# Optimization experiments

Measured on AMD Instinct MI355X. Metric: run time of the kernel, lower is better.

Reference implementation:

```python
import jax, jax.numpy as jnp
import numpy as np

NH, WIN = 8, 7  # num_head, window


def _ln(x, w, b, eps=1e-6):
    mu = x.mean(-1, keepdims=True)
    var = ((x - mu) ** 2).mean(-1, keepdims=True)
    return (x - mu) / jnp.sqrt(var + eps) * w + b


def _dwconv(x, w, b):
    # x: (B,C,H,W), w: (C,1,7,7) depthwise, pad 3
    y = jax.lax.conv_general_dilated(
        x, w, (1, 1), ((3, 3), (3, 3)),
        dimension_numbers=('NCHW', 'OIHW', 'NCHW'),
        feature_group_count=x.shape[1])
    return y + b[None, :, None, None]


def _forward(x, x_e, norm_w, norm_b, norme_w, norme_b,
             rr1_w, rr1_b, rr2_w, rr2_b, rr3_w, rr3_b, conv_w, conv_b,
             la1_w, la1_b, la2_w, la2_b, lac1_w, lac1_b, lac2_w, lac2_b,
             fc1_w, fc2_w, la3_w, la3_b,
             kv_w, kv_b, q_w, q_b, proj_w, proj_b, proje_w, proje_b):
    B, H, W, C = x.shape
    hd = C // NH // 2  # head dim of half-width attention
    xn = _ln(x, norm_w, norm_b)
    xen = _ln(x_e, norme_w, norme_b)

    # local_rr branch: gated depthwise-conv mixing (C channels)
    rr1 = xn @ rr1_w + rr1_b
    rr2 = xn @ rr2_w + rr2_b
    rr2 = _dwconv(rr2.transpose(0, 3, 1, 2), conv_w, conv_b).transpose(0, 2, 3, 1)
    rr2 = rr2 @ rr3_w + rr3_b
    local_rr = rr1 * rr2  # (B,H,W,C)

    # LocalAttentionRGBT branch -> (B,H,W,C//2)
    rgb = (xn @ la1_w + la1_b).transpose(0, 3, 1, 2)   # (B,C/2,H,W)
    t = (xen @ la2_w + la2_b).transpose(0, 3, 1, 2)
    co = _dwconv(rgb * t, lac1_w, lac1_b)
    di = _dwconv(jnp.abs(rgb - t), lac2_w, lac2_b)
    co_di = jnp.concatenate([co, di], 1).transpose(0, 2, 3, 1)  # (B,H,W,C)
    amap = co_di.mean(-1, keepdims=True)                         # (B,H,W,1)
    dot = (amap * co_di).sum((1, 2), keepdims=True)              # (B,1,1,C)
    n1 = jnp.sqrt((amap ** 2).sum((1, 2), keepdims=True))        # (B,1,1,1)
    n2 = jnp.sqrt((co_di ** 2).sum((1, 2), keepdims=True))       # (B,1,1,C)
    cos = dot / (n1 * n2 + 1e-6)
    attc = jax.nn.sigmoid(jax.nn.gelu(cos @ fc1_w, approximate=False) @ fc2_w)
    local_rx = (co_di * attc) @ la3_w + la3_b  # (B,H,W,C/2)

    # global pooled attention: 49 queries vs full H*W keys, C/2 wide
    kv = (xn @ kv_w + kv_b).reshape(B, H * W, 2, NH, hd).transpose(2, 0, 3, 1, 4)
    k, v = kv[0], kv[1]  # (B,NH,HW,hd)
    rx = jnp.concatenate([xn, xen], -1)  # (B,H,W,3C/2)
    ph, pw = H // WIN, W // WIN  # exact adaptive pool (H,W divisible by 7)
    rx_pool = rx.reshape(B, WIN, ph, WIN, pw, rx.shape[-1]).mean((2, 4))  # (B,7,7,3C/2)
    q = (rx_pool @ q_w + q_b).reshape(B, WIN * WIN, NH, hd).transpose(0, 2, 1, 3)
    attn = jax.nn.softmax((q * hd ** -0.5) @ k.transpose(0, 1, 3, 2), axis=-1)  # (B,NH,49,HW)
    g = (attn @ v).reshape(B, NH, WIN, WIN, hd).transpose(0, 1, 4, 2, 3).reshape(B, C // 2, WIN, WIN)
    g = jax.image.resize(g, (B, C // 2, H, W), method='bilinear').transpose(0, 2, 3, 1)

    xc = jnp.concatenate([local_rr, g, local_rx], -1)  # (B,H,W,2C)
    out_e = xc @ proje_w + proje_b  # (B,H,W,C/2)
    out = xc @ proj_w + proj_b      # (B,H,W,C)
    return out, out_e


def setup_inputs() -> dict:
    C = 128
    B, H, W = 8, 112, 112
    ks = iter(jax.random.split(jax.random.key(0), 24))

    def w(shape):
        return jax.random.normal(next(ks), shape, jnp.float32) * 0.05

    inp = {
        'x': jax.random.normal(next(ks), (B, H, W, C), jnp.float32),
        'x_e': jax.random.normal(next(ks), (B, H, W, C // 2), jnp.float32),
        'norm_w': jnp.ones((C,), jnp.float32), 'norm_b': jnp.zeros((C,), jnp.float32),
        'norme_w': jnp.ones((C // 2,), jnp.float32), 'norme_b': jnp.zeros((C // 2,), jnp.float32),
        'rr1_w': w((C, C)), 'rr1_b': jnp.zeros((C,), jnp.float32),
        'rr2_w': w((C, C)), 'rr2_b': jnp.zeros((C,), jnp.float32),
        'rr3_w': w((C, C)), 'rr3_b': jnp.zeros((C,), jnp.float32),
        'conv_w': w((C, 1, 7, 7)), 'conv_b': jnp.zeros((C,), jnp.float32),
        'la1_w': w((C, C // 2)), 'la1_b': jnp.zeros((C // 2,), jnp.float32),
        'la2_w': w((C // 2, C // 2)), 'la2_b': jnp.zeros((C // 2,), jnp.float32),
        'lac1_w': w((C // 2, 1, 7, 7)), 'lac1_b': jnp.zeros((C // 2,), jnp.float32),
        'lac2_w': w((C // 2, 1, 7, 7)), 'lac2_b': jnp.zeros((C // 2,), jnp.float32),
        'fc1_w': w((C, C // 8)), 'fc2_w': w((C // 8, C)),
        'la3_w': w((C, C // 2)), 'la3_b': jnp.zeros((C // 2,), jnp.float32),
        'kv_w': w((C, C)), 'kv_b': jnp.zeros((C,), jnp.float32),
        'q_w': w((3 * C // 2, C // 2)), 'q_b': jnp.zeros((C // 2,), jnp.float32),
        'proj_w': w((2 * C, C)), 'proj_b': jnp.zeros((C,), jnp.float32),
        'proje_w': w((2 * C, C // 2)), 'proje_b': jnp.zeros((C // 2,), jnp.float32),
    }
    return inp


def reference(x, x_e, norm_w, norm_b, norme_w, norme_b,
              rr1_w, rr1_b, rr2_w, rr2_b, rr3_w, rr3_b, conv_w, conv_b,
              la1_w, la1_b, la2_w, la2_b, lac1_w, lac1_b, lac2_w, lac2_b,
              fc1_w, fc2_w, la3_w, la3_b,
              kv_w, kv_b, q_w, q_b, proj_w, proj_b, proje_w, proje_b):
    return _forward(x, x_e, norm_w, norm_b, norme_w, norme_b,
                    rr1_w, rr1_b, rr2_w, rr2_b, rr3_w, rr3_b, conv_w, conv_b,
                    la1_w, la1_b, la2_w, la2_b, lac1_w, lac1_b, lac2_w, lac2_b,
                    fc1_w, fc2_w, la3_w, la3_b,
                    kv_w, kv_b, q_w, q_b, proj_w, proj_b, proje_w, proje_b)
```

## Files before the change

kernel.cpp:

```cpp
#include <hip/hip_runtime.h>
#include <math.h>

#define N_POS 100352
#define HW    12544

typedef unsigned short bf16_t;
typedef __attribute__((ext_vector_type(8))) short bf16x8;
typedef __attribute__((ext_vector_type(4))) float f32x4;

__device__ __forceinline__ bf16_t f2b(float f){
  unsigned u = __builtin_bit_cast(unsigned, f);
  unsigned r = (u + 0x7fffu + ((u >> 16) & 1u)) >> 16;
  return (bf16_t)r;
}
__device__ __forceinline__ float b2f(bf16_t h){
  unsigned u = ((unsigned)h) << 16;
  return __builtin_bit_cast(float, u);
}
__device__ __forceinline__ float blo(unsigned u){
  return __builtin_bit_cast(float, u << 16);
}
__device__ __forceinline__ float bhi(unsigned u){
  return __builtin_bit_cast(float, u & 0xffff0000u);
}

__global__ void zero_kernel(float* p, int n){
  int i = blockIdx.x*256 + threadIdx.x;
  if (i < n) p[i] = 0.f;
}

struct WJob { const float* src; bf16_t* dst; int K; int ldw; int n0; };
struct WJobs { WJob j[14]; };
__global__ void wtrans_kernel(WJobs js){
  WJob job = js.j[blockIdx.x];
  int t = threadIdx.x;
  int n = t & 63, k0 = t >> 6;
  for (int k = k0; k < job.K; k += 4)
    job.dst[(size_t)n*job.K + k] = f2b(job.src[(size_t)k*job.ldw + job.n0 + n]);
}

__global__ __launch_bounds__(256) void ln128_kernel(const float* __restrict__ in,
    const float* __restrict__ w, const float* __restrict__ b, bf16_t* __restrict__ out){
  int row  = blockIdx.x*4 + (threadIdx.x >> 6);
  int lane = threadIdx.x & 63;
  const float* p = in + (size_t)row*128;
  float2 v = *(const float2*)(p + lane*2);
  float s = v.x + v.y;
  #pragma unroll
  for (int o = 1; o < 64; o <<= 1) s += __shfl_xor(s, o);
  float mu = s * (1.0f/128.0f);
  float dx = v.x - mu, dy = v.y - mu;
  float q = dx*dx + dy*dy;
  #pragma unroll
  for (int o = 1; o < 64; o <<= 1) q += __shfl_xor(q, o);
  float rs = rsqrtf(q * (1.0f/128.0f) + 1e-6f);
  int c = lane*2;
  ushort2 o2;
  o2.x = f2b(dx*rs*w[c]   + b[c]);
  o2.y = f2b(dy*rs*w[c+1] + b[c+1]);
  *(ushort2*)(out + (size_t)row*128 + c) = o2;
}

__global__ __launch_bounds__(256) void ln64_kernel(const float* __restrict__ in,
    const float* __restrict__ w, const float* __restrict__ b, bf16_t* __restrict__ out){
  int row  = blockIdx.x*4 + (threadIdx.x >> 6);
  int lane = threadIdx.x & 63;
  float v = in[(size_t)row*64 + lane];
  float s = v;
  #pragma unroll
  for (int o = 1; o < 64; o <<= 1) s += __shfl_xor(s, o);
  float mu = s * (1.0f/64.0f);
  float d = v - mu;
  float q = d*d;
  #pragma unroll
  for (int o = 1; o < 64; o <<= 1) q += __shfl_xor(q, o);
  float rs = rsqrtf(q * (1.0f/64.0f) + 1e-6f);
  out[(size_t)row*64 + lane] = f2b(d*rs*w[lane] + b[lane]);
}

struct MTile {
  const bf16_t* Wt;
  const float* bias;
  void* out;
  const bf16_t* mult;
  int ldo; int ldm; int out_fp32;
};
struct MGemmParams {
  const bf16_t* A; const float* scale;
  int lda; int K; int rowsPerB; int ntiles;
  MTile tiles[8];
};

__global__ __launch_bounds__(256) void mgemm(MGemmParams p){
  __shared__ short As[128*72];
  __shared__ short Ws[64*72];
  const int tid = threadIdx.x;
  const int bid = blockIdx.x;
  const int xcd = bid & 7;
  const int j = bid >> 3;
  const int ti = j % p.ntiles;
  const int rb = (j / p.ntiles) * 8 + xcd;
  const MTile tile = p.tiles[ti];
  const int row0 = rb * 128;
  const int lane = tid & 63, wv = tid >> 6;
  const int wm = wv * 32;
  const int fm = lane & 15;
  const int quad = lane >> 4;
  f32x4 acc[2][4];
  #pragma unroll
  for (int mi = 0; mi < 2; mi++)
    #pragma unroll
    for (int ni = 0; ni < 4; ni++) acc[mi][ni] = (f32x4)0.f;
  const float* scale = p.scale ? (p.scale + (size_t)(row0 / p.rowsPerB) * p.K) : (const float*)0;

  const int sr = tid & 127, sq = tid >> 7;
  const int wn = tid & 63,  wq = tid >> 6;

  for (int k0 = 0; k0 < p.K; k0 += 64) {
    {
      const bf16_t* src = p.A + (size_t)(row0 + sr)*p.lda + k0 + sq*32;
      short* dst = &As[sr*72 + sq*32];
      if (!scale) {
        #pragma unroll
        for (int i = 0; i < 4; i++)
          *(uint4*)(dst + i*8) = *(const uint4*)(src + i*8);
      } else {
        const float* sc = scale + k0 + sq*32;
        #pragma unroll
        for (int i = 0; i < 32; i++) dst[i] = (short)f2b(b2f(src[i]) * sc[i]);
      }
    }
    {
      const bf16_t* src = tile.Wt + (size_t)wn*p.K + k0 + wq*16;
      short* dst = &Ws[wn*72 + wq*16];
      *(uint4*)dst       = *(const uint4*)src;
      *(uint4*)(dst + 8) = *(const uint4*)(src + 8);
    }
    __syncthreads();
    #pragma unroll
    for (int ks = 0; ks < 2; ks++) {
      int kb = ks*32 + quad*8;
      bf16x8 af0 = *(const bf16x8*)&As[(wm + fm)*72 + kb];
      bf16x8 af1 = *(const bf16x8*)&As[(wm + 16 + fm)*72 + kb];
      bf16x8 bfr[4];
      #pragma unroll
      for (int ni = 0; ni < 4; ni++) bfr[ni] = *(const bf16x8*)&Ws[(ni*16 + fm)*72 + kb];
      #pragma unroll
      for (int ni = 0; ni < 4; ni++) {
        acc[0][ni] = __builtin_amdgcn_mfma_f32_16x16x32_bf16(af0, bfr[ni], acc[0][ni], 0, 0, 0);
        acc[1][ni] = __builtin_amdgcn_mfma_f32_16x16x32_bf16(af1, bfr[ni], acc[1][ni], 0, 0, 0);
      }
    }
    __syncthreads();
  }
  #pragma unroll
  for (int mi = 0; mi < 2; mi++) {
    #pragma unroll
    for (int ni = 0; ni < 4; ni++) {
      int col = ni*16 + fm;
      float bias = tile.bias[col];
      #pragma unroll
      for (int r = 0; r < 4; r++) {
        int row = row0 + wm + mi*16 + quad*4 + r;
        float val = acc[mi][ni][r] + bias;
        if (tile.mult) val *= b2f(tile.mult[(size_t)row*tile.ldm + col]);
        if (tile.out_fp32) ((float*)tile.out)[(size_t)row*tile.ldo + col] = val;
        else ((bf16_t*)tile.out)[(size_t)row*tile.ldo + col] = f2b(val);
      }
    }
  }
}

__global__ __launch_bounds__(256) void dwconv128_kernel(const bf16_t* __restrict__ in,
    const float* __restrict__ cw, const float* __restrict__ cb, bf16_t* __restrict__ out){
  __shared__ float wsm[49*128];
  int t = threadIdx.x;
  for (int i = t; i < 6272; i += 256) {
    int ch = i & 127, k = i >> 7;
    wsm[k*128 + ch] = cw[ch*49 + k];
  }
  __syncthreads();
  int c = (t & 63) * 2;
  int wv = t >> 6;
  int blk = blockIdx.x;
  int xs = blk % 14; int tmp = blk / 14;
  int yg = tmp % 14; int b = tmp / 14;
  int y0 = yg*8 + wv*2;
  int x0 = xs*8;
  float2 bias; bias.x = cb[c]; bias.y = cb[c+1];
  float2 acc0[8], acc1[8];
  #pragma unroll
  for (int i = 0; i < 8; i++) { acc0[i] = bias; acc1[i] = bias; }
  for (int r = 0; r < 8; r++) {
    int yy = y0 + r - 3;
    if ((unsigned)yy >= 112u) continue;
    const bf16_t* row = in + ((size_t)(b*112+yy)*112)*128 + c;
    unsigned u[14];
    #pragma unroll
    for (int i = 0; i < 14; i++) {
      int xx = x0 + i - 3;
      u[i] = ((unsigned)xx < 112u) ? *(const unsigned*)(row + (size_t)xx*128) : 0u;
    }
    float va[14], vb[14];
    #pragma unroll
    for (int i = 0; i < 14; i++) { va[i] = blo(u[i]); vb[i] = bhi(u[i]); }
    if (r < 7) {
      #pragma unroll
      for (int kx = 0; kx < 7; kx++) {
        float2 w = *(const float2*)&wsm[(r*7+kx)*128 + c];
        #pragma unroll
        for (int i = 0; i < 8; i++) {
          acc0[i].x = fmaf(w.x, va[i+kx], acc0[i].x);
          acc0[i].y = fmaf(w.y, vb[i+kx], acc0[i].y);
        }
      }
    }
    if (r >= 1) {
      #pragma unroll
      for (int kx = 0; kx < 7; kx++) {
        float2 w = *(const float2*)&wsm[((r-1)*7+kx)*128 + c];
        #pragma unroll
        for (int i = 0; i < 8; i++) {
          acc1[i].x = fmaf(w.x, va[i+kx], acc1[i].x);
          acc1[i].y = fmaf(w.y, vb[i+kx], acc1[i].y);
        }
      }
    }
  }
  size_t r0 = (size_t)(b*112+y0)*112 + x0;
  #pragma unroll
  for (int i = 0; i < 8; i++) {
    unsigned o0 = (unsigned)f2b(acc0[i].x) | ((unsigned)f2b(acc0[i].y) << 16);
    unsigned o1 = (unsigned)f2b(acc1[i].x) | ((unsigned)f2b(acc1[i].y) << 16);
    *(unsigned*)(out + (r0+i)*128 + c)       = o0;
    *(unsigned*)(out + (r0+112+i)*128 + c)   = o1;
  }
}

__global__ __launch_bounds__(256) void dwconv_codi_kernel(
    const bf16_t* __restrict__ rgb, const bf16_t* __restrict__ tb,
    const float* __restrict__ w1, const float* __restrict__ b1,
    const float* __restrict__ w2, const float* __restrict__ b2,
    bf16_t* __restrict__ out){
  __shared__ float wsm[49*128];
  int t = threadIdx.x;
  for (int i = t; i < 3136; i += 256) {
    int ch = i & 63, k = i >> 6;
    wsm[k*128 + ch]      = w1[ch*49 + k];
    wsm[k*128 + 64 + ch] = w2[ch*49 + k];
  }
  __syncthreads();
  int c = (t & 31) * 2;
  int wv = t >> 5;
  int blk = blockIdx.x;
  int xs = blk % 14; int tmp = blk / 14;
  int yg = tmp % 7; int b = tmp / 7;
  int y0 = yg*16 + wv*2;
  int x0 = xs*8;
  float2 bco; bco.x = b1[c]; bco.y = b1[c+1];
  float2 bdi; bdi.x = b2[c]; bdi.y = b2[c+1];
  float2 aco0[8], aco1[8], adi0[8], adi1[8];
  #pragma unroll
  for (int i = 0; i < 8; i++) { aco0[i] = bco; aco1[i] = bco; adi0[i] = bdi; adi1[i] = bdi; }
  for (int r = 0; r < 8; r++) {
    int yy = y0 + r - 3;
    if ((unsigned)yy >= 112u) continue;
    const bf16_t* rrow = rgb + ((size_t)(b*112+yy)*112)*64 + c;
    const bf16_t* trow = tb  + ((size_t)(b*112+yy)*112)*64 + c;
    unsigned ru[14], tu[14];
    #pragma unroll
    for (int i = 0; i < 14; i++) {
      int xx = x0 + i - 3;
      bool ok = (unsigned)xx < 112u;
      ru[i] = ok ? *(const unsigned*)(rrow + (size_t)xx*64) : 0u;
      tu[i] = ok ? *(const unsigned*)(trow + (size_t)xx*64) : 0u;
    }
    float p0[14], p1[14], d0[14], d1[14];
    #pragma unroll
    for (int i = 0; i < 14; i++) {
      float a0 = blo(ru[i]), a1 = bhi(ru[i]);
      float t0 = blo(tu[i]), t1 = bhi(tu[i]);
      p0[i] = a0*t0; p1[i] = a1*t1;
      d0[i] = fabsf(a0-t0); d1[i] = fabsf(a1-t1);
    }
    if (r < 7) {
      #pragma unroll
      for (int kx = 0; kx < 7; kx++) {
        int k = r*7+kx;
        float2 wc = *(const float2*)&wsm[k*128 + c];
        float2 wd = *(const float2*)&wsm[k*128 + 64 + c];
        #pragma unroll
        for (int i = 0; i < 8; i++) {
          aco0[i].x = fmaf(wc.x, p0[i+kx], aco0[i].x);
          aco0[i].y = fmaf(wc.y, p1[i+kx], aco0[i].y);
          adi0[i].x = fmaf(wd.x, d0[i+kx], adi0[i].x);
          adi0[i].y = fmaf(wd.y, d1[i+kx], adi0[i].y);
        }
      }
    }
    if (r >= 1) {
      #pragma unroll
      for (int kx = 0; kx < 7; kx++) {
        int k = (r-1)*7+kx;
        float2 wc = *(const float2*)&wsm[k*128 + c];
        float2 wd = *(const float2*)&wsm[k*128 + 64 + c];
        #pragma unroll
        for (int i = 0; i < 8; i++) {
          aco1[i].x = fmaf(wc.x, p0[i+kx], aco1[i].x);
          aco1[i].y = fmaf(wc.y, p1[i+kx], aco1[i].y);
          adi1[i].x = fmaf(wd.x, d0[i+kx], adi1[i].x);
          adi1[i].y = fmaf(wd.y, d1[i+kx], adi1[i].y);
        }
      }
    }
  }
  size_t r0 = (size_t)(b*112+y0)*112 + x0;
  #pragma unroll
  for (int i = 0; i < 8; i++) {
    unsigned oc0 = (unsigned)f2b(aco0[i].x) | ((unsigned)f2b(aco0[i].y) << 16);
    unsigned od0 = (unsigned)f2b(adi0[i].x) | ((unsigned)f2b(adi0[i].y) << 16);
    unsigned oc1 = (unsigned)f2b(aco1[i].x) | ((unsigned)f2b(aco1[i].y) << 16);
    unsigned od1 = (unsigned)f2b(adi1[i].x) | ((unsigned)f2b(adi1[i].y) << 16);
    *(unsigned*)(out + (r0+i)*128 + c)            = oc0;
    *(unsigned*)(out + (r0+i)*128 + 64 + c)       = od0;
    *(unsigned*)(out + (r0+112+i)*128 + c)        = oc1;
    *(unsigned*)(out + (r0+112+i)*128 + 64 + c)   = od1;
  }
}

__global__ __launch_bounds__(256) void reduce_kernel(const bf16_t* __restrict__ codi,
    float* __restrict__ dotb, float* __restrict__ n1sq, float* __restrict__ n2sq){
  int blk = blockIdx.x;
  int b = blk / 49, seg = blk % 49;
  int lane = threadIdx.x & 63, w = threadIdx.x >> 6;
  int c = lane*2;
  float d0=0,d1=0,s0=0,s1=0,a1=0;
  for (int i = 0; i < 64; i++) {
    int row = b*HW + seg*256 + w*64 + i;
    ushort2 v2 = *(const ushort2*)(codi + (size_t)row*128 + c);
    float vx = b2f(v2.x), vy = b2f(v2.y);
    float rs = vx + vy;
    #pragma unroll
    for (int o = 1; o < 64; o <<= 1) rs += __shfl_xor(rs, o);
    float amap = rs * (1.0f/128.0f);
    d0 += amap*vx; d1 += amap*vy;
    s0 += vx*vx;   s1 += vy*vy;
    if (lane == 0) a1 += amap*amap;
  }
  atomicAdd(&dotb[b*128+c],   d0); atomicAdd(&dotb[b*128+c+1], d1);
  atomicAdd(&n2sq[b*128+c],   s0); atomicAdd(&n2sq[b*128+c+1], s1);
  if (lane == 0) atomicAdd(&n1sq[b], a1);
}

__global__ __launch_bounds__(128) void attc_kernel(const float* __restrict__ dotb,
    const float* __restrict__ n1sq, const float* __restrict__ n2sq,
    const float* __restrict__ fc1, const float* __restrict__ fc2, float* __restrict__ attc){
  __shared__ float scos[128];
  __shared__ float sh[16];
  int t = threadIdx.x;
  int b = blockIdx.x;
  {
    float n1 = sqrtf(n1sq[b]);
    float n2 = sqrtf(n2sq[b*128+t]);
    scos[t] = dotb[b*128+t] / (n1*n2 + 1e-6f);
  }
  __syncthreads();
  if (t < 16) {
    float h = 0;
    for (int c = 0; c < 128; c++) h += scos[c]*fc1[c*16+t];
    sh[t] = h * 0.5f * (1.0f + erff(h*0.70710678118654752f));
  }
  __syncthreads();
  {
    float a = 0;
    for (int j = 0; j < 16; j++) a += sh[j]*fc2[j*128+t];
    attc[b*128+t] = 1.0f/(1.0f + __expf(-a));
  }
}

__global__ void pool_kernel(const bf16_t* __restrict__ xn, const bf16_t* __restrict__ xen,
                            float* __restrict__ pool){
  int cellb = blockIdx.x;
  int py = blockIdx.y;
  int c = threadIdx.x;
  int b = cellb / 49, cell = cellb % 49;
  int wy = cell / 7, wx = cell % 7;
  float s = 0;
  for (int i = py*2; i < py*2+2; i++)
    for (int j = 0; j < 16; j++) {
      int y = wy*16+i, x = wx*16+j;
      size_t row = (size_t)(b*112+y)*112 + x;
      s += (c < 128) ? b2f(xn[row*128 + c]) : b2f(xen[row*64 + (c-128)]);
    }
  atomicAdd(&pool[(size_t)cellb*192 + c], s);
}

__global__ void qproj_kernel(const float* __restrict__ pool, const float* __restrict__ qw,
                             const float* __restrict__ qb, float* __restrict__ qbuf){
  int cellb = blockIdx.x;
  int j = threadIdx.x;
  float s = qb[j];
  for (int c = 0; c < 192; c++)
    s += pool[(size_t)cellb*192 + c] * (1.0f/256.0f) * qw[c*64 + j];
  qbuf[(size_t)cellb*64 + j] = s * 0.35355339059327373f;
}

__global__ __launch_bounds__(256) void attn_kernel(const float* __restrict__ qbuf,
    const bf16_t* __restrict__ kv, float* __restrict__ part){
  __shared__ float qs[392];
  __shared__ float ks[256*8];
  __shared__ float vs[256*8];
  int t = threadIdx.x;
  int blk = blockIdx.x;
  int b = blk >> 7, nh = (blk >> 4) & 7, sp = blk & 15;
  for (int i = t; i < 392; i += 256)
    qs[i] = qbuf[(size_t)(b*49 + (i>>3))*64 + nh*8 + (i&7)];
  __syncthreads();
  int lane = t & 63, w = t >> 6;
  int qq = lane < 49 ? lane : 0;
  float4 qa = *(const float4*)&qs[qq*8];
  float4 qb4 = *(const float4*)&qs[qq*8+4];
  float m = -1e30f, l = 0.f;
  float4 acca = make_float4(0,0,0,0), accb = make_float4(0,0,0,0);
  const int base = sp * 784;
  uint4 kr, vr;
  {
    size_t rb = ((size_t)(b*HW + base + t))*128 + nh*8;
    kr = *(const uint4*)(kv + rb);
    vr = *(const uint4*)(kv + rb + 64);
  }
  for (int c0 = 0; c0 < 784; c0 += 256) {
    int cnt = 784 - c0 < 256 ? 784 - c0 : 256;
    __syncthreads();
    if (t < cnt) {
      const bf16_t* kp = (const bf16_t*)&kr;
      const bf16_t* vp = (const bf16_t*)&vr;
      float4 k0 = make_float4(b2f(kp[0]), b2f(kp[1]), b2f(kp[2]), b2f(kp[3]));
      float4 k1 = make_float4(b2f(kp[4]), b2f(kp[5]), b2f(kp[6]), b2f(kp[7]));
      float4 v0 = make_float4(b2f(vp[0]), b2f(vp[1]), b2f(vp[2]), b2f(vp[3]));
      float4 v1 = make_float4(b2f(vp[4]), b2f(vp[5]), b2f(vp[6]), b2f(vp[7]));
      *(float4*)&ks[t*8]   = k0; *(float4*)&ks[t*8+4] = k1;
      *(float4*)&vs[t*8]   = v0; *(float4*)&vs[t*8+4] = v1;
    }
    __syncthreads();
    int c1 = c0 + 256;
    if (c1 < 784) {
      int cnt1 = 784 - c1 < 256 ? 784 - c1 : 256;
      if (t < cnt1) {
        size_t rb = ((size_t)(b*HW + base + c1 + t))*128 + nh*8;
        kr = *(const uint4*)(kv + rb);
        vr = *(const uint4*)(kv + rb + 64);
      }
    }
    int s0 = w*64;
    int n = cnt - s0; if (n < 0) n = 0; if (n > 64) n = 64;
    for (int i = 0; i < n; i += 16) {
      float s[16];
      #pragma unroll
      for (int j = 0; j < 16; j++) {
        const float* kp = &ks[(s0+i+j)*8];
        float4 ka = *(const float4*)kp, kb = *(const float4*)(kp+4);
        s[j] = qa.x*ka.x + qa.y*ka.y + qa.z*ka.z + qa.w*ka.w
             + qb4.x*kb.x + qb4.y*kb.y + qb4.z*kb.z + qb4.w*kb.w;
      }
      float t8[8];
      #pragma unroll
      for (int j = 0; j < 8; j++) t8[j] = fmaxf(s[2*j], s[2*j+1]);
      float t4a = fmaxf(t8[0], t8[1]), t4b = fmaxf(t8[2], t8[3]);
      float t4c = fmaxf(t8[4], t8[5]), t4d = fmaxf(t8[6], t8[7]);
      float mx = fmaxf(fmaxf(t4a, t4b), fmaxf(t4c, t4d));
      float mn = fmaxf(m, mx);
      float corr = __expf(m - mn);
      float p[16];
      #pragma unroll
      for (int j = 0; j < 16; j++) p[j] = __expf(s[j] - mn);
      float u8[8];
      #pragma unroll
      for (int j = 0; j < 8; j++) u8[j] = p[2*j] + p[2*j+1];
      float u4a = u8[0]+u8[1], u4b = u8[2]+u8[3], u4c = u8[4]+u8[5], u4d = u8[6]+u8[7];
      float lsum = (u4a+u4b) + (u4c+u4d);
      l = fmaf(l, corr, lsum);
      float4 sva = make_float4(0,0,0,0), svb = make_float4(0,0,0,0);
      #pragma unroll
      for (int j = 0; j < 16; j++) {
        const float* vp = &vs[(s0+i+j)*8];
        float4 va = *(const float4*)vp, vb = *(const float4*)(vp+4);
        sva.x = fmaf(p[j], va.x, sva.x); sva.y = fmaf(p[j], va.y, sva.y);
        sva.z = fmaf(p[j], va.z, sva.z); sva.w = fmaf(p[j], va.w, sva.w);
        svb.x = fmaf(p[j], vb.x, svb.x); svb.y = fmaf(p[j], vb.y, svb.y);
        svb.z = fmaf(p[j], vb.z, svb.z); svb.w = fmaf(p[j], vb.w, svb.w);
      }
      acca.x = fmaf(acca.x, corr, sva.x); acca.y = fmaf(acca.y, corr, sva.y);
      acca.z = fmaf(acca.z, corr, sva.z); acca.w = fmaf(acca.w, corr, sva.w);
      accb.x = fmaf(accb.x, corr, svb.x); accb.y = fmaf(accb.y, corr, svb.y);
      accb.z = fmaf(accb.z, corr, svb.z); accb.w = fmaf(accb.w, corr, svb.w);
      m = mn;
    }
  }
  __syncthreads();
  if (lane < 49) {
    float* rp = &vs[((size_t)w*49 + lane)*10];
    rp[0] = m; rp[1] = l;
    rp[2] = acca.x; rp[3] = acca.y; rp[4] = acca.z; rp[5] = acca.w;
    rp[6] = accb.x; rp[7] = accb.y; rp[8] = accb.z; rp[9] = accb.w;
  }
  __syncthreads();
  if (t < 49) {
    float M = -1e30f;
    #pragma unroll
    for (int w4 = 0; w4 < 4; w4++) M = fmaxf(M, vs[(w4*49 + t)*10]);
    float L = 0, a[8] = {0,0,0,0,0,0,0,0};
    #pragma unroll
    for (int w4 = 0; w4 < 4; w4++) {
      const float* rp = &vs[(w4*49 + t)*10];
      float c = __expf(rp[0] - M);
      L += rp[1]*c;
      #pragma unroll
      for (int d = 0; d < 8; d++) a[d] += rp[2+d]*c;
    }
    size_t idx = ((size_t)blk*49 + t)*10;
    part[idx] = M; part[idx+1] = L;
    #pragma unroll
    for (int d = 0; d < 8; d++) part[idx+2+d] = a[d];
  }
}

__global__ void merge_kernel(const float* __restrict__ part, float* __restrict__ gsm){
  int g = blockIdx.x*64 + threadIdx.x;
  if (g >= 3136) return;
  int b = g / 392, r = g % 392, nh = r / 49, q = r % 49;
  int blkbase = b*128 + nh*16;
  float M = -1e30f;
  for (int sp = 0; sp < 16; sp++)
    M = fmaxf(M, part[((size_t)(blkbase+sp)*49 + q)*10]);
  float L = 0, a[8] = {0,0,0,0,0,0,0,0};
  for (int sp = 0; sp < 16; sp++) {
    size_t idx = ((size_t)(blkbase+sp)*49 + q)*10;
    float c = __expf(part[idx] - M);
    L += part[idx+1]*c;
    #pragma unroll
    for (int d = 0; d < 8; d++) a[d] += part[idx+2+d]*c;
  }
  #pragma unroll
  for (int d = 0; d < 8; d++)
    gsm[(size_t)(b*49+q)*64 + nh*8 + d] = a[d]/L;
}

__global__ __launch_bounds__(256) void f2_kernel(const float* __restrict__ gsm,
                                                 bf16_t* __restrict__ xc){
  int gidx = blockIdx.x*256 + threadIdx.x;
  int r = gidx >> 6, cc = gidx & 63;
  int b = r / HW, rem = r % HW, y = rem / 112, x = rem % 112;
  float fy = fminf(fmaxf((y + 0.5f)*0.0625f - 0.5f, 0.f), 6.f);
  float fx = fminf(fmaxf((x + 0.5f)*0.0625f - 0.5f, 0.f), 6.f);
  int y0 = (int)fy, x0 = (int)fx;
  float wy = fy - y0, wx = fx - x0;
  int y1 = y0+1 < 6 ? y0+1 : 6, x1 = x0+1 < 6 ? x0+1 : 6;
  const float* gb = gsm + (size_t)b*49*64 + cc;
  float g00 = gb[(y0*7+x0)*64], g01 = gb[(y0*7+x1)*64];
  float g10 = gb[(y1*7+x0)*64], g11 = gb[(y1*7+x1)*64];
  xc[(size_t)r*256 + 128 + cc] =
      f2b((1-wy)*((1-wx)*g00 + wx*g01) + wy*((1-wx)*g10 + wx*g11));
}

extern "C" void kernel_launch(void* const* d_in, const int* in_sizes, int n_in,
                              void* d_out, int out_size, void* d_ws, size_t ws_size,
                              hipStream_t stream) {
  const float* x      = (const float*)d_in[0];
  const float* x_e    = (const float*)d_in[1];
  const float* norm_w = (const float*)d_in[2];
  const float* norm_b = (const float*)d_in[3];
  const float* norme_w= (const float*)d_in[4];
  const float* norme_b= (const float*)d_in[5];
  const float* rr1_w  = (const float*)d_in[6];
  const float* rr1_b  = (const float*)d_in[7];
  const float* rr2_w  = (const float*)d_in[8];
  const float* rr2_b  = (const float*)d_in[9];
  const float* rr3_w  = (const float*)d_in[10];
  const float* rr3_b  = (const float*)d_in[11];
  const float* conv_w = (const float*)d_in[12];
  const float* conv_b = (const float*)d_in[13];
  const float* la1_w  = (const float*)d_in[14];
  const float* la1_b  = (const float*)d_in[15];
  const float* la2_w  = (const float*)d_in[16];
  const float* la2_b  = (const float*)d_in[17];
  const float* lac1_w = (const float*)d_in[18];
  const float* lac1_b = (const float*)d_in[19];
  const float* lac2_w = (const float*)d_in[20];
  const float* lac2_b = (const float*)d_in[21];
  const float* fc1_w  = (const float*)d_in[22];
  const float* fc2_w  = (const float*)d_in[23];
  const float* la3_w  = (const float*)d_in[24];
  const float* la3_b  = (const float*)d_in[25];
  const float* kv_w   = (const float*)d_in[26];
  const float* kv_b   = (const float*)d_in[27];
  const float* q_w    = (const float*)d_in[28];
  const float* q_b    = (const float*)d_in[29];
  const float* proj_w = (const float*)d_in[30];
  const float* proj_b = (const float*)d_in[31];
  const float* proje_w= (const float*)d_in[32];
  const float* proje_b= (const float*)d_in[33];

  const size_t N = N_POS;
  bf16_t* rr1   = (bf16_t*)d_ws;
  bf16_t* xnbuf = rr1 + N*128;
  bf16_t* kvbuf = xnbuf + N*128;
  bf16_t* xcbuf = kvbuf + N*128;
  float* pool = (float*)(xcbuf + N*256);
  float* qbuf = pool + 75264;
  float* part = qbuf + 25088;
  float* gsm  = part + 1003520;
  float* dotb = gsm  + 25088;
  float* n1sq = dotb + 1024;
  float* n2sq = n1sq + 8;
  float* attc = n2sq + 1024;
  bf16_t* wtab = (bf16_t*)(attc + 1024);

  bf16_t* xn = xnbuf;
  bf16_t* convout = xnbuf;
  bf16_t* kv = kvbuf;
  bf16_t* codi = kvbuf;
  bf16_t* rr2a = xcbuf;
  bf16_t* rgb  = xcbuf + N*128;
  bf16_t* xen  = xcbuf + N*192;
  bf16_t* xc   = xcbuf;
  float* outp = (float*)d_out;
  float* oute = outp + N*128;

  bf16_t* rr1t0 = wtab;            bf16_t* rr1t1 = wtab + 8192;
  bf16_t* rr2t0 = wtab + 16384;    bf16_t* rr2t1 = wtab + 24576;
  bf16_t* la1t  = wtab + 32768;
  bf16_t* kvt0  = wtab + 40960;    bf16_t* kvt1  = wtab + 49152;
  bf16_t* la2t  = wtab + 57344;
  bf16_t* rr3t0 = wtab + 61440;    bf16_t* rr3t1 = wtab + 69632;
  bf16_t* la3t  = wtab + 77824;
  bf16_t* projt0= wtab + 86016;    bf16_t* projt1= wtab + 102400;
  bf16_t* projet= wtab + 118784;

  zero_kernel<<<(75264+255)/256, 256, 0, stream>>>(pool, 75264);
  zero_kernel<<<9, 256, 0, stream>>>(dotb, 2056);
  {
    WJobs js;
    js.j[0]  = {rr1_w,  rr1t0, 128, 128,   0};
    js.j[1]  = {rr1_w,  rr1t1, 128, 128,  64};
    js.j[2]  = {rr2_w,  rr2t0, 128, 128,   0};
    js.j[3]  = {rr2_w,  rr2t1, 128, 128,  64};
    js.j[4]  = {la1_w,  la1t,  128,  64,   0};
    js.j[5]  = {kv_w,   kvt0,  128, 128,   0};
    js.j[6]  = {kv_w,   kvt1,  128, 128,  64};
    js.j[7]  = {la2_w,  la2t,   64,  64,   0};
    js.j[8]  = {rr3_w,  rr3t0, 128, 128,   0};
    js.j[9]  = {rr3_w,  rr3t1, 128, 128,  64};
    js.j[10] = {la3_w,  la3t,  128,  64,   0};
    js.j[11] = {proj_w, projt0,256, 128,   0};
    js.j[12] = {proj_w, projt1,256, 128,  64};
    js.j[13] = {proje_w,projet,256,  64,   0};
    wtrans_kernel<<<14, 256, 0, stream>>>(js);
  }
  ln128_kernel<<<N_POS/4, 256, 0, stream>>>(x, norm_w, norm_b, xn);
  ln64_kernel <<<N_POS/4, 256, 0, stream>>>(x_e, norme_w, norme_b, xen);
  pool_kernel<<<dim3(392,8), 192, 0, stream>>>(xn, xen, pool);
  qproj_kernel<<<392, 64, 0, stream>>>(pool, q_w, q_b, qbuf);
  {
    MGemmParams p; p.A = xn; p.scale = 0; p.lda = 128; p.K = 128; p.rowsPerB = HW; p.ntiles = 7;
    p.tiles[0] = {rr1t0, rr1_b,    rr1,     0, 128, 0, 0};
    p.tiles[1] = {rr1t1, rr1_b+64, rr1+64,  0, 128, 0, 0};
    p.tiles[2] = {rr2t0, rr2_b,    rr2a,    0, 128, 0, 0};
    p.tiles[3] = {rr2t1, rr2_b+64, rr2a+64, 0, 128, 0, 0};
    p.tiles[4] = {la1t,  la1_b,    rgb,     0,  64, 0, 0};
    p.tiles[5] = {kvt0,  kv_b,     kv,      0, 128, 0, 0};
    p.tiles[6] = {kvt1,  kv_b+64,  kv+64,   0, 128, 0, 0};
    mgemm<<<8*7*98, 256, 0, stream>>>(p);
  }
  attn_kernel<<<1024, 256, 0, stream>>>(qbuf, kv, part);
  merge_kernel<<<49, 64, 0, stream>>>(part, gsm);
  {
    MGemmParams p; p.A = xen; p.scale = 0; p.lda = 64; p.K = 64; p.rowsPerB = HW; p.ntiles = 1;
    p.tiles[0] = {la2t, la2_b, xen, 0, 64, 0, 0};
    mgemm<<<8*1*98, 256, 0, stream>>>(p);
  }
  dwconv_codi_kernel<<<8*7*14, 256, 0, stream>>>(rgb, xen, lac1_w, lac1_b, lac2_w, lac2_b, codi);
  dwconv128_kernel<<<8*14*14, 256, 0, stream>>>(rr2a, conv_w, conv_b, convout);
  {
    MGemmParams p; p.A = convout; p.scale = 0; p.lda = 128; p.K = 128; p.rowsPerB = HW; p.ntiles = 2;
    p.tiles[0] = {rr3t0, rr3_b,    xc,    rr1,    256, 128, 0};
    p.tiles[1] = {rr3t1, rr3_b+64, xc+64, rr1+64, 256, 128, 0};
    mgemm<<<8*2*98, 256, 0, stream>>>(p);
  }
  reduce_kernel<<<392, 256, 0, stream>>>(codi, dotb, n1sq, n2sq);
  attc_kernel<<<8, 128, 0, stream>>>(dotb, n1sq, n2sq, fc1_w, fc2_w, attc);
  {
    MGemmParams p; p.A = codi; p.scale = attc; p.lda = 128; p.K = 128; p.rowsPerB = HW; p.ntiles = 1;
    p.tiles[0] = {la3t, la3_b, xc + 192, 0, 256, 0, 0};
    mgemm<<<8*1*98, 256, 0, stream>>>(p);
  }
  f2_kernel<<<25088, 256, 0, stream>>>(gsm, xc);
  {
    MGemmParams p; p.A = xc; p.scale = 0; p.lda = 256; p.K = 256; p.rowsPerB = HW; p.ntiles = 3;
    p.tiles[0] = {projt0, proj_b,    outp,    0, 128, 0, 1};
    p.tiles[1] = {projt1, proj_b+64, outp+64, 0, 128, 0, 1};
    p.tiles[2] = {projet, proje_b,   oute,    0,  64, 0, 1};
    mgemm<<<8*3*98, 256, 0, stream>>>(p);
  }
}
```

Baseline: 596.3 us.

## Keep A row-block resident in LDS and loop over N tiles per block

The multi-tile GEMM becomes a templated kernel in which each block loads its full-K A row block into shared memory once and then iterates over all output column tiles. Previously each block handled one tile and reloaded A for every tile. The next weight chunk is prefetched into registers while MFMAs run on the current one, and K and the tile sizes are now compile-time constants. In exchange each block does more serial work, the grid is smaller, and larger LDS use may limit occupancy.

```diff
diff --git a/kernel.cpp b/kernel.cpp
--- a/kernel.cpp
+++ b/kernel.cpp
@@ -86,86 +86,128 @@
   int ldo; int ldm; int out_fp32;
 };
 struct MGemmParams {
-  const bf16_t* A; const float* scale;
-  int lda; int K; int rowsPerB; int ntiles;
+  const bf16_t* A;
+  const float* scale;
+  int rowsPerB; int ntiles;
   MTile tiles[8];
 };
 
-__global__ __launch_bounds__(256) void mgemm(MGemmParams p){
-  __shared__ short As[128*72];
-  __shared__ short Ws[64*72];
+template<int BM, int K>
+__global__ __launch_bounds__(256, 3) void mgemm_mt(MGemmParams p){
+  constexpr int KC  = (K > 128) ? 128 : K;
+  constexpr int NKC = K / KC;
+  constexpr int LDA = K + 8;
+  constexpr int LDW = KC + 8;
+  constexpr int MI  = BM / 64;
+  constexpr int RQ  = K / 8;
+  constexpr int RQC = KC / 8;
+  constexpr int NC  = BM * K / 2048;
+  constexpr int NW  = 64 * KC / 2048;
+  __shared__ short As[BM * LDA];
+  __shared__ short Ws[64 * LDW];
   const int tid = threadIdx.x;
-  const int bid = blockIdx.x;
-  const int xcd = bid & 7;
-  const int j = bid >> 3;
-  const int ti = j % p.ntiles;
-  const int rb = (j / p.ntiles) * 8 + xcd;
-  const MTile tile = p.tiles[ti];
-  const int row0 = rb * 128;
+  const int row0 = blockIdx.x * BM;
   const int lane = tid & 63, wv = tid >> 6;
-  const int wm = wv * 32;
-  const int fm = lane & 15;
-  const int quad = lane >> 4;
-  f32x4 acc[2][4];
-  #pragma unroll
-  for (int mi = 0; mi < 2; mi++)
-    #pragma unroll
-    for (int ni = 0; ni < 4; ni++) acc[mi][ni] = (f32x4)0.f;
-  const float* scale = p.scale ? (p.scale + (size_t)(row0 / p.rowsPerB) * p.K) : (const float*)0;
-
-  const int sr = tid & 127, sq = tid >> 7;
-  const int wn = tid & 63,  wq = tid >> 6;
-
-  for (int k0 = 0; k0 < p.K; k0 += 64) {
-    {
-      const bf16_t* src = p.A + (size_t)(row0 + sr)*p.lda + k0 + sq*32;
-      short* dst = &As[sr*72 + sq*32];
-      if (!scale) {
-        #pragma unroll
-        for (int i = 0; i < 4; i++)
-          *(uint4*)(dst + i*8) = *(const uint4*)(src + i*8);
-      } else {
-        const float* sc = scale + k0 + sq*32;
-        #pragma unroll
-        for (int i = 0; i < 32; i++) dst[i] = (short)f2b(b2f(src[i]) * sc[i]);
-      }
-    }
-    {
-      const bf16_t* src = tile.Wt + (size_t)wn*p.K + k0 + wq*16;
-      short* dst = &Ws[wn*72 + wq*16];
-      *(uint4*)dst       = *(const uint4*)src;
-      *(uint4*)(dst + 8) = *(const uint4*)(src + 8);
-    }
-    __syncthreads();
-    #pragma unroll
-    for (int ks = 0; ks < 2; ks++) {
-      int kb = ks*32 + quad*8;
-      bf16x8 af0 = *(const bf16x8*)&As[(wm + fm)*72 + kb];
-      bf16x8 af1 = *(const bf16x8*)&As[(wm + 16 + fm)*72 + kb];
-      bf16x8 bfr[4];
-      #pragma unroll
-      for (int ni = 0; ni < 4; ni++) bfr[ni] = *(const bf16x8*)&Ws[(ni*16 + fm)*72 + kb];
+  const int wm = wv * (BM / 4);
+  const int fm = lane & 15, quad = lane >> 4;
+
+  {
+    const bf16_t* srcA = p.A + (size_t)row0 * K;
+    if (!p.scale) {
+      #pragma unroll
+      for (int i = 0; i < NC; i++) {
+        int c = tid + i*256;
+        *(uint4*)&As[(c/RQ)*LDA + (c%RQ)*8] = *(const uint4*)(srcA + c*8);
+      }
+    } else {
+      const float* sc = p.scale + (size_t)(row0 / p.rowsPerB) * K;
+      #pragma unroll
+      for (int i = 0; i < NC; i++) {
+        int c = tid + i*256;
+        int kq = c % RQ;
+        uint4 v = *(const uint4*)(srcA + c*8);
+        const bf16_t* vp = (const bf16_t*)&v;
+        short tmp[8];
+        #pragma unroll
+        for (int j = 0; j < 8; j++) tmp[j] = (short)f2b(b2f(vp[j]) * sc[kq*8 + j]);
+        *(uint4*)&As[(c/RQ)*LDA + kq*8] = *(const uint4*)tmp;
+      }
+    }
+  }
+  {
+    const bf16_t* srcW = p.tiles[0].Wt;
+    #pragma unroll
+    for (int i = 0; i < NW; i++) {
+      int c = tid + i*256;
+      *(uint4*)&Ws[(c/RQC)*LDW + (c%RQC)*8] = *(const uint4*)(srcW + (c/RQC)*K + (c%RQC)*8);
+    }
+  }
+  __syncthreads();
+
+  const int nt = p.ntiles;
+  for (int t = 0; t < nt; t++) {
+    const MTile tile = p.tiles[t];
+    f32x4 acc[MI][4];
+    #pragma unroll
+    for (int mi = 0; mi < MI; mi++)
+      #pragma unroll
+      for (int ni = 0; ni < 4; ni++) acc[mi][ni] = (f32x4)0.f;
+
+    #pragma unroll
+    for (int kc = 0; kc < NKC; kc++) {
+      const bool hasNext = (kc+1 < NKC) || (t+1 < nt);
+      const bf16_t* nW = (kc+1 < NKC) ? (tile.Wt + (kc+1)*KC)
+                        : ((t+1 < nt) ? p.tiles[t+1].Wt : (const bf16_t*)0);
+      uint4 rw[NW];
+      if (hasNext) {
+        #pragma unroll
+        for (int i = 0; i < NW; i++) {
+          int c = tid + i*256;
+          rw[i] = *(const uint4*)(nW + (c/RQC)*K + (c%RQC)*8);
+        }
+      }
+      #pragma unroll
+      for (int ks = 0; ks < KC/32; ks++) {
+        int kbw = ks*32 + quad*8;
+        int kba = kc*KC + kbw;
+        bf16x8 af[MI];
+        #pragma unroll
+        for (int mi = 0; mi < MI; mi++)
+          af[mi] = *(const bf16x8*)&As[(wm + mi*16 + fm)*LDA + kba];
+        bf16x8 bfr[4];
+        #pragma unroll
+        for (int ni = 0; ni < 4; ni++)
+          bfr[ni] = *(const bf16x8*)&Ws[(ni*16 + fm)*LDW + kbw];
+        #pragma unroll
+        for (int ni = 0; ni < 4; ni++)
+          #pragma unroll
+          for (int mi = 0; mi < MI; mi++)
+            acc[mi][ni] = __builtin_amdgcn_mfma_f32_16x16x32_bf16(af[mi], bfr[ni], acc[mi][ni], 0, 0, 0);
+      }
+      if (hasNext) {
+        __syncthreads();
+        #pragma unroll
+        for (int i = 0; i < NW; i++) {
+          int c = tid + i*256;
+          *(uint4*)&Ws[(c/RQC)*LDW + (c%RQC)*8] = rw[i];
+        }
+        __syncthreads();
+      }
+    }
+    #pragma unroll
+    for (int mi = 0; mi < MI; mi++) {
       #pragma unroll
       for (int ni = 0; ni < 4; ni++) {
-        acc[0][ni] = __builtin_amdgcn_mfma_f32_16x16x32_bf16(af0, bfr[ni], acc[0][ni], 0, 0, 0);
-        acc[1][ni] = __builtin_amdgcn_mfma_f32_16x16x32_bf16(af1, bfr[ni], acc[1][ni], 0, 0, 0);
-      }
-    }
-    __syncthreads();
-  }
-  #pragma unroll
-  for (int mi = 0; mi < 2; mi++) {
-    #pragma unroll
-    for (int ni = 0; ni < 4; ni++) {
-      int col = ni*16 + fm;
-      float bias = tile.bias[col];
-      #pragma unroll
-      for (int r = 0; r < 4; r++) {
-        int row = row0 + wm + mi*16 + quad*4 + r;
-        float val = acc[mi][ni][r] + bias;
-        if (tile.mult) val *= b2f(tile.mult[(size_t)row*tile.ldm + col]);
-        if (tile.out_fp32) ((float*)tile.out)[(size_t)row*tile.ldo + col] = val;
-        else ((bf16_t*)tile.out)[(size_t)row*tile.ldo + col] = f2b(val);
+        int col = ni*16 + fm;
+        float bias = tile.bias[col];
+        #pragma unroll
+        for (int r = 0; r < 4; r++) {
+          int row = row0 + wm + mi*16 + quad*4 + r;
+          float val = acc[mi][ni][r] + bias;
+          if (tile.mult) val *= b2f(tile.mult[(size_t)row*tile.ldm + col]);
+          if (tile.out_fp32) ((float*)tile.out)[(size_t)row*tile.ldo + col] = val;
+          else ((bf16_t*)tile.out)[(size_t)row*tile.ldo + col] = f2b(val);
+        }
       }
     }
   }
@@ -662,7 +704,7 @@
   pool_kernel<<<dim3(392,8), 192, 0, stream>>>(xn, xen, pool);
   qproj_kernel<<<392, 64, 0, stream>>>(pool, q_w, q_b, qbuf);
   {
-    MGemmParams p; p.A = xn; p.scale = 0; p.lda = 128; p.K = 128; p.rowsPerB = HW; p.ntiles = 7;
+    MGemmParams p; p.A = xn; p.scale = 0; p.rowsPerB = HW; p.ntiles = 7;
     p.tiles[0] = {rr1t0, rr1_b,    rr1,     0, 128, 0, 0};
     p.tiles[1] = {rr1t1, rr1_b+64, rr1+64,  0, 128, 0, 0};
     p.tiles[2] = {rr2t0, rr2_b,    rr2a,    0, 128, 0, 0};
@@ -670,36 +712,36 @@
     p.tiles[4] = {la1t,  la1_b,    rgb,     0,  64, 0, 0};
     p.tiles[5] = {kvt0,  kv_b,     kv,      0, 128, 0, 0};
     p.tiles[6] = {kvt1,  kv_b+64,  kv+64,   0, 128, 0, 0};
-    mgemm<<<8*7*98, 256, 0, stream>>>(p);
+    mgemm_mt<128,128><<<N_POS/128, 256, 0, stream>>>(p);
   }
   attn_kernel<<<1024, 256, 0, stream>>>(qbuf, kv, part);
   merge_kernel<<<49, 64, 0, stream>>>(part, gsm);
   {
-    MGemmParams p; p.A = xen; p.scale = 0; p.lda = 64; p.K = 64; p.rowsPerB = HW; p.ntiles = 1;
+    MGemmParams p; p.A = xen; p.scale = 0; p.rowsPerB = HW; p.ntiles = 1;
     p.tiles[0] = {la2t, la2_b, xen, 0, 64, 0, 0};
-    mgemm<<<8*1*98, 256, 0, stream>>>(p);
+    mgemm_mt<128,64><<<N_POS/128, 256, 0, stream>>>(p);
   }
   dwconv_codi_kernel<<<8*7*14, 256, 0, stream>>>(rgb, xen, lac1_w, lac1_b, lac2_w, lac2_b, codi);
   dwconv128_kernel<<<8*14*14, 256, 0, stream>>>(rr2a, conv_w, conv_b, convout);
   {
-    MGemmParams p; p.A = convout; p.scale = 0; p.lda = 128; p.K = 128; p.rowsPerB = HW; p.ntiles = 2;
+    MGemmParams p; p.A = convout; p.scale = 0; p.rowsPerB = HW; p.ntiles = 2;
     p.tiles[0] = {rr3t0, rr3_b,    xc,    rr1,    256, 128, 0};
     p.tiles[1] = {rr3t1, rr3_b+64, xc+64, rr1+64, 256, 128, 0};
-    mgemm<<<8*2*98, 256, 0, stream>>>(p);
+    mgemm_mt<128,128><<<N_POS/128, 256, 0, stream>>>(p);
   }
   reduce_kernel<<<392, 256, 0, stream>>>(codi, dotb, n1sq, n2sq);
   attc_kernel<<<8, 128, 0, stream>>>(dotb, n1sq, n2sq, fc1_w, fc2_w, attc);
   {
-    MGemmParams p; p.A = codi; p.scale = attc; p.lda = 128; p.K = 128; p.rowsPerB = HW; p.ntiles = 1;
+    MGemmParams p; p.A = codi; p.scale = attc; p.rowsPerB = HW; p.ntiles = 1;
     p.tiles[0] = {la3t, la3_b, xc + 192, 0, 256, 0, 0};
-    mgemm<<<8*1*98, 256, 0, stream>>>(p);
+    mgemm_mt<128,128><<<N_POS/128, 256, 0, stream>>>(p);
   }
   f2_kernel<<<25088, 256, 0, stream>>>(gsm, xc);
   {
-    MGemmParams p; p.A = xc; p.scale = 0; p.lda = 256; p.K = 256; p.rowsPerB = HW; p.ntiles = 3;
+    MGemmParams p; p.A = xc; p.scale = 0; p.rowsPerB = HW; p.ntiles = 3;
     p.tiles[0] = {projt0, proj_b,    outp,    0, 128, 0, 1};
     p.tiles[1] = {projt1, proj_b+64, outp+64, 0, 128, 0, 1};
     p.tiles[2] = {projet, proje_b,   oute,    0,  64, 0, 1};
-    mgemm<<<8*3*98, 256, 0, stream>>>(p);
-  }
-}
+    mgemm_mt<64,256><<<N_POS/64, 256, 0, stream>>>(p);
+  }
+}
```

Measured after the change: 649.6 us. 1.09x slower.
